# Kernel tuning notes

Hardware: AMD Instinct MI355X
Metric: run time of the kernel (lower is better)

The kernel has to match this reference:

```python
import jax, jax.numpy as jnp
import numpy as np

D_MODEL = 1024
NUM_HEADS = 16
HEAD_DIM = D_MODEL // NUM_HEADS
THETA = 10000.0
B, S = 1, 2048


def setup_inputs() -> dict:
    key = jax.random.key(0)
    ks = jax.random.split(key, 7)
    sc = 0.02
    return {
        "query": jax.random.normal(ks[0], (B, S, D_MODEL), jnp.float32),
        "key": jax.random.normal(ks[1], (B, S, D_MODEL), jnp.float32),
        "value": jax.random.normal(ks[2], (B, S, D_MODEL), jnp.float32),
        "qkv_w": jax.random.normal(ks[3], (3 * D_MODEL, D_MODEL), jnp.float32) * sc,
        "qkv_b": jax.random.normal(ks[4], (3 * D_MODEL,), jnp.float32) * sc,
        "out_w": jax.random.normal(ks[5], (D_MODEL, D_MODEL), jnp.float32) * sc,
        "out_b": jax.random.normal(ks[6], (D_MODEL,), jnp.float32) * sc,
    }


def _rope_cos_sin(seq_len, head_dim, dtype):
    # freqs_for='lang': inv_freq = theta^(-2i/d), i = 0..d/2-1
    inv_freq = 1.0 / (THETA ** (jnp.arange(0, head_dim, 2, dtype=jnp.float32) / head_dim))
    t = jnp.arange(seq_len, dtype=jnp.float32)
    freqs = jnp.outer(t, inv_freq)                      # [S, d/2]
    emb = jnp.concatenate([freqs, freqs], axis=-1)      # [S, d] (non-interleaved)
    return jnp.cos(emb).astype(dtype), jnp.sin(emb).astype(dtype)


def _rotate_half(x):
    half = x.shape[-1] // 2
    return jnp.concatenate([-x[..., half:], x[..., :half]], axis=-1)


def reference(query, key, value, qkv_w, qkv_b, out_w, out_b):
    # NOTE: module computes q,k,v all from `query` (key/value args unused).
    b, s, d = query.shape
    qkv = query @ qkv_w.T + qkv_b                       # [B,S,3D]
    qkv = qkv.reshape(b, s, 3, NUM_HEADS, HEAD_DIM)
    qkv = jnp.transpose(qkv, (2, 0, 3, 1, 4))           # [3,B,H,S,hd]
    q, k, v = qkv[0], qkv[1], qkv[2]

    cos, sin = _rope_cos_sin(s, HEAD_DIM, query.dtype)  # [S,hd]
    q = q * cos + _rotate_half(q) * sin
    k = k * cos + _rotate_half(k) * sin

    scale = 1.0 / np.sqrt(HEAD_DIM)
    scores = jnp.einsum('bhqd,bhkd->bhqk', q, k) * scale
    attn = jax.nn.softmax(scores, axis=-1)
    ctx = jnp.einsum('bhqk,bhkd->bhqd', attn, v)        # [B,H,S,hd]
    ctx = jnp.transpose(ctx, (0, 2, 1, 3)).reshape(b, s, d)
    return ctx @ out_w.T + out_b
```

## Files before the change

kernel.cpp:

```cpp
#include <hip/hip_runtime.h>
#include <math.h>
#include <stdint.h>

#define SEQ 2048
#define DM  1024
#define NH  16
#define HD  64
#define TRI 3072
#define NSPLIT 4

typedef _Float16 half8 __attribute__((ext_vector_type(8)));
typedef _Float16 half4 __attribute__((ext_vector_type(4)));
typedef __fp16 fp16x2 __attribute__((ext_vector_type(2)));
typedef float f32x4 __attribute__((ext_vector_type(4)));

#define GLOAD_LDS16(g, l)                                       \
  __builtin_amdgcn_global_load_lds(                             \
      (__attribute__((address_space(1))) void*)(g),             \
      (__attribute__((address_space(3))) void*)(l), 16, 0, 0)

#define QSCALE 0.18033688011112042f

__global__ __launch_bounds__(256)
void cvt3(const float* __restrict__ s1, const float* __restrict__ s2,
          const float* __restrict__ s3, _Float16* __restrict__ d1,
          _Float16* __restrict__ d2, _Float16* __restrict__ d3,
          float2* __restrict__ tab, int n1, int n2) {
  int b = blockIdx.x;
  if (b >= 6144) {
    int i = (b - 6144) * 256 + threadIdx.x;
    int s = i >> 5, d = i & 31;
    float inv = exp2f((float)d * -0.4152410118609203f);
    float ang = (float)s * inv;
    float sn, cs;
    sincosf(ang, &sn, &cs);
    tab[i] = make_float2(cs, sn);
    return;
  }
  int i = (b * 256 + threadIdx.x) * 4;
  const float* s; _Float16* d;
  if (i < n1)            { s = s1; d = d1; }
  else if (i < n1 + n2)  { s = s2; d = d2; i -= n1; }
  else                   { s = s3; d = d3; i -= n1 + n2; }
  float4 v = *(const float4*)(s + i);
  union { _Float16 h[4]; uint2 u; } pk;
  pk.h[0] = (_Float16)v.x; pk.h[1] = (_Float16)v.y;
  pk.h[2] = (_Float16)v.z; pk.h[3] = (_Float16)v.w;
  *(uint2*)(d + i) = pk.u;
}

__global__ __launch_bounds__(256)
void gemm_qkv(const _Float16* __restrict__ A, const _Float16* __restrict__ B,
              const float* __restrict__ bias, const float2* __restrict__ tab,
              _Float16* __restrict__ Qo, _Float16* __restrict__ Ko,
              _Float16* __restrict__ Vo) {
  constexpr int K = DM;
  __shared__ _Float16 As[2][64 * 32];
  __shared__ _Float16 Bs[2][128 * 32];

  const int t = threadIdx.x, lane = t & 63, wv = t >> 6;
  const int l15 = lane & 15, l4 = lane >> 4;
  const int wr = wv >> 1, wc = wv & 1;
  const int bm = blockIdx.y * 64, bn = blockIdx.x * 128;

  auto stage = [&](int buf, int k0) {
    {
      int c = t;
      GLOAD_LDS16(A + (size_t)(bm + (c >> 2)) * K + k0 + (c & 3) * 8,
                  (char*)&As[buf][wv * 512]);
    }
    #pragma unroll
    for (int i = 0; i < 2; ++i) {
      int c = t + i * 256;
      GLOAD_LDS16(B + (size_t)(bn + (c >> 2)) * K + k0 + (c & 3) * 8,
                  (char*)&Bs[buf][(i * 256 + wv * 64) * 8]);
    }
  };

  f32x4 acc[2][4] = {};
  stage(0, 0);
  __syncthreads();

  const int nk = K / 32;
  for (int s = 0; s < nk; ++s) {
    int cur = s & 1;
    if (s + 1 < nk) stage(cur ^ 1, (s + 1) * 32);
    half8 af[2], bf[4];
    #pragma unroll
    for (int mf = 0; mf < 2; ++mf)
      af[mf] = *(const half8*)&As[cur][(wr * 32 + mf * 16 + l15) * 32 + l4 * 8];
    #pragma unroll
    for (int nf = 0; nf < 4; ++nf)
      bf[nf] = *(const half8*)&Bs[cur][(wc * 64 + nf * 16 + l15) * 32 + l4 * 8];
    __builtin_amdgcn_s_setprio(1);
    #pragma unroll
    for (int mf = 0; mf < 2; ++mf)
      #pragma unroll
      for (int nf = 0; nf < 4; ++nf)
        acc[mf][nf] = __builtin_amdgcn_mfma_f32_16x16x32_f16(
            af[mf], bf[nf], acc[mf][nf], 0, 0, 0);
    __builtin_amdgcn_s_setprio(0);
    __syncthreads();
  }

  const int sec = bn >> 10;
  float bv[4];
  #pragma unroll
  for (int nf = 0; nf < 4; ++nf) bv[nf] = bias[bn + wc * 64 + nf * 16 + l15];

  if (sec == 0) {
    #pragma unroll
    for (int mf = 0; mf < 2; ++mf)
      #pragma unroll
      for (int r = 0; r < 4; ++r) {
        int row = bm + wr * 32 + mf * 16 + l4 * 4 + r;
        float v0 = acc[mf][0][r] + bv[0];
        float v1 = acc[mf][1][r] + bv[1];
        float v2 = acc[mf][2][r] + bv[2];
        float v3 = acc[mf][3][r] + bv[3];
        float2 cs0 = tab[row * 32 + l15];
        float2 cs1 = tab[row * 32 + 16 + l15];
        float a0 = (v0 * cs0.x - v2 * cs0.y) * QSCALE;
        float a2 = (v2 * cs0.x + v0 * cs0.y) * QSCALE;
        float a1 = (v1 * cs1.x - v3 * cs1.y) * QSCALE;
        float a3 = (v3 * cs1.x + v1 * cs1.y) * QSCALE;
        _Float16* cr = Qo + (size_t)row * DM + bn + wc * 64 + l15;
        cr[0]  = (_Float16)a0; cr[16] = (_Float16)a1;
        cr[32] = (_Float16)a2; cr[48] = (_Float16)a3;
      }
  } else if (sec == 1) {
    const int hh = ((bn - 1024) >> 6) + wc;
    const int e = l15 & 7, hi = l15 >> 3;
    #pragma unroll
    for (int mf = 0; mf < 2; ++mf)
      #pragma unroll
      for (int r = 0; r < 4; ++r) {
        int row = bm + wr * 32 + mf * 16 + l4 * 4 + r;
        float v0 = acc[mf][0][r] + bv[0];
        float v1 = acc[mf][1][r] + bv[1];
        float v2 = acc[mf][2][r] + bv[2];
        float v3 = acc[mf][3][r] + bv[3];
        float2 cs0 = tab[row * 32 + l15];
        float2 cs1 = tab[row * 32 + 16 + l15];
        float a0 = v0 * cs0.x - v2 * cs0.y;
        float a2 = v2 * cs0.x + v0 * cs0.y;
        float a1 = v1 * cs1.x - v3 * cs1.y;
        float a3 = v3 * cs1.x + v1 * cs1.y;
        int kk = row & 63, kseg = row >> 6;
        int hkk = (kk & 3) | ((kk >> 1) & 4);
        size_t base = ((size_t)(hh * 32 + kseg) * 64 + kk) * 64;
        Ko[base + (((0 + hi) ^ hkk) * 8) + e] = (_Float16)a0;
        Ko[base + (((2 + hi) ^ hkk) * 8) + e] = (_Float16)a1;
        Ko[base + (((4 + hi) ^ hkk) * 8) + e] = (_Float16)a2;
        Ko[base + (((6 + hi) ^ hkk) * 8) + e] = (_Float16)a3;
      }
  } else {
    const int hh = ((bn - 2048) >> 6) + wc;
    #pragma unroll
    for (int mf = 0; mf < 2; ++mf) {
      int row0 = bm + wr * 32 + mf * 16 + l4 * 4;
      int kk0 = row0 & 63, kseg = row0 >> 6;
      #pragma unroll
      for (int nf = 0; nf < 4; ++nf) {
        int d = nf * 16 + l15;
        union { _Float16 hh4[4]; uint2 u; } pk;
        #pragma unroll
        for (int r = 0; r < 4; ++r)
          pk.hh4[r] = (_Float16)(acc[mf][nf][r] + bv[nf]);
        size_t off = ((size_t)(hh * 32 + kseg) * 64 + d) * 64 +
                     (((kk0 >> 3) ^ (d & 7)) * 8) + (kk0 & 7);
        *(uint2*)(Vo + off) = pk.u;
      }
    }
  }
}

__global__ __launch_bounds__(256)
void gemm_out(const _Float16* __restrict__ A, const _Float16* __restrict__ B,
              const float* __restrict__ bias, float* __restrict__ C) {
  constexpr int K = DM, N = DM;
  __shared__ _Float16 As[2][64 * 32];
  __shared__ _Float16 Bs[2][128 * 32];

  const int t = threadIdx.x, lane = t & 63, wv = t >> 6;
  const int l15 = lane & 15, l4 = lane >> 4;
  const int wr = wv >> 1, wc = wv & 1;
  const int bm = blockIdx.y * 64, bn = blockIdx.x * 128;

  auto stage = [&](int buf, int k0) {
    {
      int c = t;
      GLOAD_LDS16(A + (size_t)(bm + (c >> 2)) * K + k0 + (c & 3) * 8,
                  (char*)&As[buf][wv * 512]);
    }
    #pragma unroll
    for (int i = 0; i < 2; ++i) {
      int c = t + i * 256;
      GLOAD_LDS16(B + (size_t)(bn + (c >> 2)) * K + k0 + (c & 3) * 8,
                  (char*)&Bs[buf][(i * 256 + wv * 64) * 8]);
    }
  };

  f32x4 acc[2][4] = {};
  stage(0, 0);
  __syncthreads();

  const int nk = K / 32;
  for (int s = 0; s < nk; ++s) {
    int cur = s & 1;
    if (s + 1 < nk) stage(cur ^ 1, (s + 1) * 32);
    half8 af[2], bf[4];
    #pragma unroll
    for (int mf = 0; mf < 2; ++mf)
      af[mf] = *(const half8*)&As[cur][(wr * 32 + mf * 16 + l15) * 32 + l4 * 8];
    #pragma unroll
    for (int nf = 0; nf < 4; ++nf)
      bf[nf] = *(const half8*)&Bs[cur][(wc * 64 + nf * 16 + l15) * 32 + l4 * 8];
    __builtin_amdgcn_s_setprio(1);
    #pragma unroll
    for (int mf = 0; mf < 2; ++mf)
      #pragma unroll
      for (int nf = 0; nf < 4; ++nf)
        acc[mf][nf] = __builtin_amdgcn_mfma_f32_16x16x32_f16(
            af[mf], bf[nf], acc[mf][nf], 0, 0, 0);
    __builtin_amdgcn_s_setprio(0);
    __syncthreads();
  }

  float bv[4];
  #pragma unroll
  for (int nf = 0; nf < 4; ++nf) bv[nf] = bias[bn + wc * 64 + nf * 16 + l15];
  #pragma unroll
  for (int mf = 0; mf < 2; ++mf)
    #pragma unroll
    for (int r = 0; r < 4; ++r) {
      int row = bm + wr * 32 + mf * 16 + l4 * 4 + r;
      float* cr = C + (size_t)row * N + bn + wc * 64 + l15;
      cr[0]  = acc[mf][0][r] + bv[0];
      cr[16] = acc[mf][1][r] + bv[1];
      cr[32] = acc[mf][2][r] + bv[2];
      cr[48] = acc[mf][3][r] + bv[3];
    }
}

__global__ __launch_bounds__(256)
void attn_f16(const _Float16* __restrict__ Qg, const _Float16* __restrict__ Kg,
              const _Float16* __restrict__ Vg, _Float16* __restrict__ poA,
              _Float16* __restrict__ po3, float* __restrict__ pl) {
  __shared__ _Float16 Kl[2][64 * 64];
  __shared__ _Float16 Vt[2][64 * 64];

  const int t = threadIdx.x, lane = t & 63, wv = t >> 6;
  const int l15 = lane & 15, l4 = lane >> 4;
  const int bid = blockIdx.x;
  const int c = bid & 63, qb = bid >> 6;
  const int h = c & 15, z = c >> 4;
  const int q0 = qb * 64;
  const int seg0 = z * (SEQ / NSPLIT / 64);

  const _Float16* Qp = Qg + h * HD;
  const _Float16* Kbase = Kg + (size_t)h * 32 * 4096;
  const _Float16* Vbase = Vg + (size_t)h * 32 * 4096;

  half8 qf[2];
  {
    const _Float16* qrow = Qp + (size_t)(q0 + wv * 16 + l15) * DM;
    qf[0] = *(const half8*)(qrow + l4 * 8);
    qf[1] = *(const half8*)(qrow + 32 + l4 * 8);
  }

  auto issueKV = [&](int buf, int seg) {
    const _Float16* ks = Kbase + (size_t)seg * 4096;
    const _Float16* vs = Vbase + (size_t)seg * 4096;
    GLOAD_LDS16(ks + (size_t)t * 8,         (char*)&Kl[buf][(wv * 64) * 8]);
    GLOAD_LDS16(ks + (size_t)(t + 256) * 8, (char*)&Kl[buf][(256 + wv * 64) * 8]);
    GLOAD_LDS16(vs + (size_t)t * 8,         (char*)&Vt[buf][(wv * 64) * 8]);
    GLOAD_LDS16(vs + (size_t)(t + 256) * 8, (char*)&Vt[buf][(256 + wv * 64) * 8]);
  };

  f32x4 lacc = {0.f, 0.f, 0.f, 0.f};
  f32x4 o[4] = {};

  const int hk = (l15 & 3) | (((l15 >> 2) & 1) << 2);
  const int krow = 8 * (l15 >> 2) + (l15 & 3);

  issueKV(0, seg0);

  const int NT = SEQ / NSPLIT / 64;
  #pragma unroll 2
  for (int tt = 0; tt < NT; ++tt) {
    const int cur = tt & 1;
    asm volatile("s_waitcnt vmcnt(0)" ::: "memory");
    __builtin_amdgcn_s_barrier();
    __builtin_amdgcn_sched_barrier(0);
    if (tt + 1 < NT) issueKV(cur ^ 1, seg0 + tt + 1);

    f32x4 sT[4] = {};
    __builtin_amdgcn_s_setprio(1);
    #pragma unroll
    for (int ds = 0; ds < 2; ++ds)
      #pragma unroll
      for (int m = 0; m < 4; ++m) {
        int kappa = 32 * (m >> 1) + 4 * (m & 1) + krow;
        int cb = ds * 4 + l4;
        half8 kf = *(const half8*)((char*)Kl[cur] + kappa * 128 +
                                   ((cb ^ hk) * 16));
        sT[m] = __builtin_amdgcn_mfma_f32_16x16x32_f16(kf, qf[ds], sT[m], 0, 0, 0);
      }
    __builtin_amdgcn_s_setprio(0);

    half8 pB[2];
    #pragma unroll
    for (int s2 = 0; s2 < 2; ++s2) {
      union { fp16x2 h2[4]; half8 v; } pu;
      #pragma unroll
      for (int mh = 0; mh < 2; ++mh) {
        int m = s2 * 2 + mh;
        f32x4 p;
        #pragma unroll
        for (int r = 0; r < 4; ++r) p[r] = exp2f(sT[m][r]);
        lacc += p;
        pu.h2[mh * 2 + 0] = __builtin_amdgcn_cvt_pkrtz(p[0], p[1]);
        pu.h2[mh * 2 + 1] = __builtin_amdgcn_cvt_pkrtz(p[2], p[3]);
      }
      pB[s2] = pu.v;
    }

    __builtin_amdgcn_s_setprio(1);
    #pragma unroll
    for (int s2 = 0; s2 < 2; ++s2)
      #pragma unroll
      for (int nf = 0; nf < 4; ++nf) {
        half8 va = *(const half8*)((char*)Vt[cur] + (nf * 16 + l15) * 128 +
                                   (((s2 * 4 + l4) ^ (l15 & 7)) * 16));
        o[nf] = __builtin_amdgcn_mfma_f32_16x16x32_f16(va, pB[s2], o[nf], 0, 0, 0);
      }
    __builtin_amdgcn_s_setprio(0);
  }

  float lv = (lacc[0] + lacc[1]) + (lacc[2] + lacc[3]);
  lv += __shfl_xor(lv, 16);
  lv += __shfl_xor(lv, 32);
  _Float16* pz = (z < 3) ? (poA + (size_t)z * SEQ * DM) : po3;
  {
    int row = q0 + wv * 16 + l15;
    _Float16* pr = pz + (size_t)row * DM + h * HD + l4 * 4;
    #pragma unroll
    for (int nf = 0; nf < 4; ++nf) {
      union { fp16x2 h2[2]; uint2 u; } ou;
      ou.h2[0] = __builtin_amdgcn_cvt_pkrtz(o[nf][0], o[nf][1]);
      ou.h2[1] = __builtin_amdgcn_cvt_pkrtz(o[nf][2], o[nf][3]);
      *(uint2*)(pr + nf * 16) = ou.u;
    }
  }
  if (l4 == 0) {
    int q = q0 + wv * 16 + l15;
    pl[(z * NH + h) * SEQ + q] = lv;
  }
}

__global__ __launch_bounds__(256)
void merge4(const _Float16* __restrict__ poA, const _Float16* __restrict__ po3,
            const float* __restrict__ pl, _Float16* __restrict__ ctx) {
  int e = (blockIdx.x * 256 + threadIdx.x) * 8;
  int s = e >> 10, h = (e & 1023) >> 6;
  int idx = h * SEQ + s;
  float L = pl[idx] + pl[NH * SEQ + idx] + pl[2 * NH * SEQ + idx] +
            pl[3 * NH * SEQ + idx];
  float inv = 1.0f / L;
  half8 a = *(const half8*)(poA + e);
  half8 b = *(const half8*)(poA + (size_t)SEQ * DM + e);
  half8 cc = *(const half8*)(poA + 2 * (size_t)SEQ * DM + e);
  half8 d = *(const half8*)(po3 + e);
  half8 o;
  #pragma unroll
  for (int j = 0; j < 8; ++j)
    o[j] = (_Float16)((((float)a[j] + (float)b[j]) +
                       ((float)cc[j] + (float)d[j])) * inv);
  *(half8*)(ctx + e) = o;
}

extern "C" void kernel_launch(void* const* d_in, const int* in_sizes, int n_in,
                              void* d_out, int out_size, void* d_ws, size_t ws_size,
                              hipStream_t stream) {
  const float* query = (const float*)d_in[0];
  const float* qkv_w = (const float*)d_in[3];
  const float* qkv_b = (const float*)d_in[4];
  const float* out_w = (const float*)d_in[5];
  const float* out_b = (const float*)d_in[6];
  float* out = (float*)d_out;

  char* ws = (char*)d_ws;
  _Float16* Aq   = (_Float16*)ws;
  _Float16* Wqkv = (_Float16*)(ws + (4u << 20));
  _Float16* Qb   = (_Float16*)(ws + (12u << 20));
  _Float16* Kb   = (_Float16*)(ws + (16u << 20));
  _Float16* Vb   = (_Float16*)(ws + (20u << 20));
  _Float16* ctx  = (_Float16*)(ws + (24u << 20));
  float2*   tab  = (float2*)(ws + (28u << 20));
  _Float16* Wout = (_Float16*)(ws + (28u << 20) + (512u << 10));
  float*    pl   = (float*)(ws + (30u << 20) + (512u << 10));
  _Float16* poA  = (_Float16*)ws;
  _Float16* po3  = ctx;

  cvt3<<<6400, 256, 0, stream>>>(query, qkv_w, out_w, Aq, Wqkv, Wout, tab,
                                 SEQ * DM, TRI * DM);

  gemm_qkv<<<dim3(TRI / 128, SEQ / 64), 256, 0, stream>>>(
      Aq, Wqkv, qkv_b, tab, Qb, Kb, Vb);

  attn_f16<<<(SEQ / 64) * NH * NSPLIT, 256, 0, stream>>>(
      Qb, Kb, Vb, poA, po3, pl);

  merge4<<<SEQ * DM / 8 / 256, 256, 0, stream>>>(poA, po3, pl, ctx);

  gemm_out<<<dim3(DM / 128, SEQ / 64), 256, 0, stream>>>(ctx, Wout, out_b, out);
}
```

Measured before the change: 96.90 us.

## Triple-buffer GEMM K loop and move K swizzle into attention loads

Both projection GEMMs now share one templated kernel that keeps three LDS stages in flight. It waits with vmcnt(3) and a single barrier per K step instead of double buffering with two syncthreads. K is now written row-major like Q, which replaces the scattered per-element swizzled stores, and the attention kernel applies the XOR swizzle through per-thread global offsets when it loads K tiles. The change adds 50% more LDS per GEMM block, which may lower occupancy, and the attention K loads become strided rows of 128 bytes instead of one contiguous 8 KB tile.

```diff
diff --git a/kernel.cpp b/kernel.cpp
--- a/kernel.cpp
+++ b/kernel.cpp
@@ -10,7 +10,6 @@
 #define NSPLIT 4
 
 typedef _Float16 half8 __attribute__((ext_vector_type(8)));
-typedef _Float16 half4 __attribute__((ext_vector_type(4)));
 typedef __fp16 fp16x2 __attribute__((ext_vector_type(2)));
 typedef float f32x4 __attribute__((ext_vector_type(4)));
 
@@ -49,14 +48,15 @@
   *(uint2*)(d + i) = pk.u;
 }
 
+template<int EPI, typename OutT>
 __global__ __launch_bounds__(256)
-void gemm_qkv(const _Float16* __restrict__ A, const _Float16* __restrict__ B,
-              const float* __restrict__ bias, const float2* __restrict__ tab,
-              _Float16* __restrict__ Qo, _Float16* __restrict__ Ko,
-              _Float16* __restrict__ Vo) {
+void gemm_p3(const _Float16* __restrict__ A, const _Float16* __restrict__ B,
+             const float* __restrict__ bias, const float2* __restrict__ tab,
+             OutT* __restrict__ C, _Float16* __restrict__ Ko,
+             _Float16* __restrict__ Vo, int N) {
   constexpr int K = DM;
-  __shared__ _Float16 As[2][64 * 32];
-  __shared__ _Float16 Bs[2][128 * 32];
+  __shared__ _Float16 As[3][64 * 32];
+  __shared__ _Float16 Bs[3][128 * 32];
 
   const int t = threadIdx.x, lane = t & 63, wv = t >> 6;
   const int l15 = lane & 15, l4 = lane >> 4;
@@ -79,12 +79,17 @@
 
   f32x4 acc[2][4] = {};
   stage(0, 0);
-  __syncthreads();
+  stage(1, 32);
 
   const int nk = K / 32;
   for (int s = 0; s < nk; ++s) {
-    int cur = s & 1;
-    if (s + 1 < nk) stage(cur ^ 1, (s + 1) * 32);
+    int cur = s % 3;
+    if (s + 1 < nk) asm volatile("s_waitcnt vmcnt(3)" ::: "memory");
+    else            asm volatile("s_waitcnt vmcnt(0)" ::: "memory");
+    __builtin_amdgcn_s_barrier();
+    __builtin_amdgcn_sched_barrier(0);
+    if (s + 2 < nk) stage((s + 2) % 3, (s + 2) * 32);
+
     half8 af[2], bf[4];
     #pragma unroll
     for (int mf = 0; mf < 2; ++mf)
@@ -100,37 +105,30 @@
         acc[mf][nf] = __builtin_amdgcn_mfma_f32_16x16x32_f16(
             af[mf], bf[nf], acc[mf][nf], 0, 0, 0);
     __builtin_amdgcn_s_setprio(0);
-    __syncthreads();
-  }
-
-  const int sec = bn >> 10;
+  }
+
   float bv[4];
   #pragma unroll
   for (int nf = 0; nf < 4; ++nf) bv[nf] = bias[bn + wc * 64 + nf * 16 + l15];
 
-  if (sec == 0) {
+  if (EPI == 0) {
     #pragma unroll
     for (int mf = 0; mf < 2; ++mf)
       #pragma unroll
       for (int r = 0; r < 4; ++r) {
         int row = bm + wr * 32 + mf * 16 + l4 * 4 + r;
-        float v0 = acc[mf][0][r] + bv[0];
-        float v1 = acc[mf][1][r] + bv[1];
-        float v2 = acc[mf][2][r] + bv[2];
-        float v3 = acc[mf][3][r] + bv[3];
-        float2 cs0 = tab[row * 32 + l15];
-        float2 cs1 = tab[row * 32 + 16 + l15];
-        float a0 = (v0 * cs0.x - v2 * cs0.y) * QSCALE;
-        float a2 = (v2 * cs0.x + v0 * cs0.y) * QSCALE;
-        float a1 = (v1 * cs1.x - v3 * cs1.y) * QSCALE;
-        float a3 = (v3 * cs1.x + v1 * cs1.y) * QSCALE;
-        _Float16* cr = Qo + (size_t)row * DM + bn + wc * 64 + l15;
-        cr[0]  = (_Float16)a0; cr[16] = (_Float16)a1;
-        cr[32] = (_Float16)a2; cr[48] = (_Float16)a3;
-      }
-  } else if (sec == 1) {
-    const int hh = ((bn - 1024) >> 6) + wc;
-    const int e = l15 & 7, hi = l15 >> 3;
+        OutT* cr = C + (size_t)row * N + bn + wc * 64 + l15;
+        cr[0]  = (OutT)(acc[mf][0][r] + bv[0]);
+        cr[16] = (OutT)(acc[mf][1][r] + bv[1]);
+        cr[32] = (OutT)(acc[mf][2][r] + bv[2]);
+        cr[48] = (OutT)(acc[mf][3][r] + bv[3]);
+      }
+    return;
+  }
+
+  const int sec = bn >> 10;
+  if (sec < 2) {
+    OutT* dst = (sec == 0) ? C : (OutT*)Ko;
     #pragma unroll
     for (int mf = 0; mf < 2; ++mf)
       #pragma unroll
@@ -146,13 +144,10 @@
         float a2 = v2 * cs0.x + v0 * cs0.y;
         float a1 = v1 * cs1.x - v3 * cs1.y;
         float a3 = v3 * cs1.x + v1 * cs1.y;
-        int kk = row & 63, kseg = row >> 6;
-        int hkk = (kk & 3) | ((kk >> 1) & 4);
-        size_t base = ((size_t)(hh * 32 + kseg) * 64 + kk) * 64;
-        Ko[base + (((0 + hi) ^ hkk) * 8) + e] = (_Float16)a0;
-        Ko[base + (((2 + hi) ^ hkk) * 8) + e] = (_Float16)a1;
-        Ko[base + (((4 + hi) ^ hkk) * 8) + e] = (_Float16)a2;
-        Ko[base + (((6 + hi) ^ hkk) * 8) + e] = (_Float16)a3;
+        if (sec == 0) { a0 *= QSCALE; a1 *= QSCALE; a2 *= QSCALE; a3 *= QSCALE; }
+        OutT* cr = dst + (size_t)row * DM + (bn & 1023) + wc * 64 + l15;
+        cr[0]  = (OutT)a0; cr[16] = (OutT)a1;
+        cr[32] = (OutT)a2; cr[48] = (OutT)a3;
       }
   } else {
     const int hh = ((bn - 2048) >> 6) + wc;
@@ -176,74 +171,6 @@
 }
 
 __global__ __launch_bounds__(256)
-void gemm_out(const _Float16* __restrict__ A, const _Float16* __restrict__ B,
-              const float* __restrict__ bias, float* __restrict__ C) {
-  constexpr int K = DM, N = DM;
-  __shared__ _Float16 As[2][64 * 32];
-  __shared__ _Float16 Bs[2][128 * 32];
-
-  const int t = threadIdx.x, lane = t & 63, wv = t >> 6;
-  const int l15 = lane & 15, l4 = lane >> 4;
-  const int wr = wv >> 1, wc = wv & 1;
-  const int bm = blockIdx.y * 64, bn = blockIdx.x * 128;
-
-  auto stage = [&](int buf, int k0) {
-    {
-      int c = t;
-      GLOAD_LDS16(A + (size_t)(bm + (c >> 2)) * K + k0 + (c & 3) * 8,
-                  (char*)&As[buf][wv * 512]);
-    }
-    #pragma unroll
-    for (int i = 0; i < 2; ++i) {
-      int c = t + i * 256;
-      GLOAD_LDS16(B + (size_t)(bn + (c >> 2)) * K + k0 + (c & 3) * 8,
-                  (char*)&Bs[buf][(i * 256 + wv * 64) * 8]);
-    }
-  };
-
-  f32x4 acc[2][4] = {};
-  stage(0, 0);
-  __syncthreads();
-
-  const int nk = K / 32;
-  for (int s = 0; s < nk; ++s) {
-    int cur = s & 1;
-    if (s + 1 < nk) stage(cur ^ 1, (s + 1) * 32);
-    half8 af[2], bf[4];
-    #pragma unroll
-    for (int mf = 0; mf < 2; ++mf)
-      af[mf] = *(const half8*)&As[cur][(wr * 32 + mf * 16 + l15) * 32 + l4 * 8];
-    #pragma unroll
-    for (int nf = 0; nf < 4; ++nf)
-      bf[nf] = *(const half8*)&Bs[cur][(wc * 64 + nf * 16 + l15) * 32 + l4 * 8];
-    __builtin_amdgcn_s_setprio(1);
-    #pragma unroll
-    for (int mf = 0; mf < 2; ++mf)
-      #pragma unroll
-      for (int nf = 0; nf < 4; ++nf)
-        acc[mf][nf] = __builtin_amdgcn_mfma_f32_16x16x32_f16(
-            af[mf], bf[nf], acc[mf][nf], 0, 0, 0);
-    __builtin_amdgcn_s_setprio(0);
-    __syncthreads();
-  }
-
-  float bv[4];
-  #pragma unroll
-  for (int nf = 0; nf < 4; ++nf) bv[nf] = bias[bn + wc * 64 + nf * 16 + l15];
-  #pragma unroll
-  for (int mf = 0; mf < 2; ++mf)
-    #pragma unroll
-    for (int r = 0; r < 4; ++r) {
-      int row = bm + wr * 32 + mf * 16 + l4 * 4 + r;
-      float* cr = C + (size_t)row * N + bn + wc * 64 + l15;
-      cr[0]  = acc[mf][0][r] + bv[0];
-      cr[16] = acc[mf][1][r] + bv[1];
-      cr[32] = acc[mf][2][r] + bv[2];
-      cr[48] = acc[mf][3][r] + bv[3];
-    }
-}
-
-__global__ __launch_bounds__(256)
 void attn_f16(const _Float16* __restrict__ Qg, const _Float16* __restrict__ Kg,
               const _Float16* __restrict__ Vg, _Float16* __restrict__ poA,
               _Float16* __restrict__ po3, float* __restrict__ pl) {
@@ -259,7 +186,7 @@
   const int seg0 = z * (SEQ / NSPLIT / 64);
 
   const _Float16* Qp = Qg + h * HD;
-  const _Float16* Kbase = Kg + (size_t)h * 32 * 4096;
+  const _Float16* Kp = Kg + h * HD;
   const _Float16* Vbase = Vg + (size_t)h * 32 * 4096;
 
   half8 qf[2];
@@ -269,11 +196,19 @@
     qf[1] = *(const half8*)(qrow + 32 + l4 * 8);
   }
 
+  int koff[2];
+  #pragma unroll
+  for (int i = 0; i < 2; ++i) {
+    int cc = t + i * 256, kk = cc >> 3, p = cc & 7;
+    int hkk = (kk & 3) | ((kk >> 1) & 4);
+    koff[i] = kk * DM + ((p ^ hkk) * 8);
+  }
+
   auto issueKV = [&](int buf, int seg) {
-    const _Float16* ks = Kbase + (size_t)seg * 4096;
+    const _Float16* ks = Kp + (size_t)seg * 64 * DM;
     const _Float16* vs = Vbase + (size_t)seg * 4096;
-    GLOAD_LDS16(ks + (size_t)t * 8,         (char*)&Kl[buf][(wv * 64) * 8]);
-    GLOAD_LDS16(ks + (size_t)(t + 256) * 8, (char*)&Kl[buf][(256 + wv * 64) * 8]);
+    GLOAD_LDS16(ks + koff[0],               (char*)&Kl[buf][(wv * 64) * 8]);
+    GLOAD_LDS16(ks + koff[1],               (char*)&Kl[buf][(256 + wv * 64) * 8]);
     GLOAD_LDS16(vs + (size_t)t * 8,         (char*)&Vt[buf][(wv * 64) * 8]);
     GLOAD_LDS16(vs + (size_t)(t + 256) * 8, (char*)&Vt[buf][(256 + wv * 64) * 8]);
   };
@@ -406,13 +341,14 @@
   cvt3<<<6400, 256, 0, stream>>>(query, qkv_w, out_w, Aq, Wqkv, Wout, tab,
                                  SEQ * DM, TRI * DM);
 
-  gemm_qkv<<<dim3(TRI / 128, SEQ / 64), 256, 0, stream>>>(
-      Aq, Wqkv, qkv_b, tab, Qb, Kb, Vb);
+  gemm_p3<1, _Float16><<<dim3(TRI / 128, SEQ / 64), 256, 0, stream>>>(
+      Aq, Wqkv, qkv_b, tab, Qb, Kb, Vb, TRI);
 
   attn_f16<<<(SEQ / 64) * NH * NSPLIT, 256, 0, stream>>>(
       Qb, Kb, Vb, poA, po3, pl);
 
   merge4<<<SEQ * DM / 8 / 256, 256, 0, stream>>>(poA, po3, pl, ctx);
 
-  gemm_out<<<dim3(DM / 128, SEQ / 64), 256, 0, stream>>>(ctx, Wout, out_b, out);
-}
+  gemm_p3<0, float><<<dim3(DM / 128, SEQ / 64), 256, 0, stream>>>(
+      ctx, Wout, out_b, nullptr, out, nullptr, nullptr, DM);
+}
```

New measurement: 93.85 us. -3.1%, faster.
